# Kernel tuning notes

Measured on AMD Instinct MI355X. Metric: run time of the kernel, lower is better.

The kernel has to match this reference:

```python
import jax, jax.numpy as jnp
import numpy as np

N_NODES = 100000
N_EDGES = 1600000
IN_DIM, HID_DIM, OUT_DIM = 128, 128, 64


def setup_inputs() -> dict:
    key = jax.random.key(0)
    k1, k2, k3, k4 = jax.random.split(key, 4)
    x = jax.random.normal(k1, (N_NODES, IN_DIM), dtype=jnp.float32)
    edge_index = jax.random.randint(k2, (2, N_EDGES), 0, N_NODES, dtype=jnp.int64)
    # Glorot-ish init for weights, zeros for biases (as in PyG GCNConv defaults)
    W1 = jax.random.normal(k3, (IN_DIM, HID_DIM), dtype=jnp.float32) * (1.0 / np.sqrt(IN_DIM))
    b1 = jnp.zeros((HID_DIM,), dtype=jnp.float32)
    W2 = jax.random.normal(k4, (HID_DIM, OUT_DIM), dtype=jnp.float32) * (1.0 / np.sqrt(HID_DIM))
    b2 = jnp.zeros((OUT_DIM,), dtype=jnp.float32)
    return {"x": x, "edge_index": edge_index, "W1": W1, "b1": b1, "W2": W2, "b2": b2}


def _build_norm(edge_index, num_nodes):
    """Add self-loops and compute symmetric GCN normalization per edge.
    Returns (src, dst, norm) with self-loops appended."""
    loops = jnp.arange(num_nodes, dtype=edge_index.dtype)
    src = jnp.concatenate([edge_index[0], loops])
    dst = jnpp_concat = jnp.concatenate([edge_index[1], loops])
    deg = jax.ops.segment_sum(jnp.ones_like(dst, dtype=jnp.float32), dst,
                              num_segments=num_nodes)
    dinv = jax.lax.rsqrt(deg)  # deg >= 1 due to self-loops
    norm = dinv[src] * dinv[dst]  # [E + N]
    return src, dst, norm


def _gcn_conv(h, W, b, src, dst, norm, num_nodes):
    h = h @ W                                   # [N, F_out]
    msg = h[src] * norm[:, None]                # gather + scale, [E+N, F_out]
    agg = jax.ops.segment_sum(msg, dst, num_segments=num_nodes)
    return agg + b


def reference(x, edge_index, W1, b1, W2, b2):
    num_nodes = x.shape[0]
    src, dst, norm = _build_norm(edge_index, num_nodes)
    h = jax.nn.relu(_gcn_conv(x, W1, b1, src, dst, norm, num_nodes))
    return _gcn_conv(h, W2, b2, src, dst, norm, num_nodes)
```

## Files before the change

### kernel.cpp

```cpp
#include <hip/hip_runtime.h>

#define NN 100000
#define NE 1600000
#define NB 782
#define NBPAD 1024
#define CAPB 3072
#define EPB 8192
#define NROWPAD 100096
#define DPAD 136
#define OPAD 72

typedef __attribute__((ext_vector_type(8))) short short8;
typedef __attribute__((ext_vector_type(4))) float f32x4;

__device__ __forceinline__ unsigned short bf16rn(float f) {
    unsigned u = __float_as_uint(f);
    return (unsigned short)((u + 0x7FFFu + ((u >> 16) & 1u)) >> 16);
}
__device__ __forceinline__ float4 bf2x4(uint2 g) {
    float4 r;
    r.x = __uint_as_float(g.x << 16);
    r.y = __uint_as_float(g.x & 0xFFFF0000u);
    r.z = __uint_as_float(g.y << 16);
    r.w = __uint_as_float(g.y & 0xFFFF0000u);
    return r;
}
__device__ __forceinline__ uint2 packbf4(float4 v) {
    uint2 u;
    u.x = (unsigned)bf16rn(v.x) | ((unsigned)bf16rn(v.y) << 16);
    u.y = (unsigned)bf16rn(v.z) | ((unsigned)bf16rn(v.w) << 16);
    return u;
}

__global__ void detect_i64_k(const unsigned* __restrict__ ei, int* __restrict__ flag) {
    unsigned w = ei[2 * threadIdx.x + 1];
    unsigned long long b = __ballot(w == 0u);
    if (threadIdx.x == 0) *flag = (b == 0xFFFFFFFFFFFFFFFFull) ? 1 : 0;
}
__device__ __forceinline__ int load_node(const void* ei, int i64, long long idx) {
    return i64 ? (int)((const long long*)ei)[idx] : ((const int*)ei)[idx];
}

__global__ void cast_bf16_k(const float* __restrict__ in, ushort* __restrict__ outb,
                            long long n4) {
    long long i = (long long)blockIdx.x * 256 + threadIdx.x;
    if (i >= n4) return;
    ((uint2*)outb)[i] = packbf4(((const float4*)in)[i]);
}

__global__ void prep_wt_k(const float* __restrict__ W1, const float* __restrict__ W2,
                          ushort* __restrict__ W1t, ushort* __restrict__ W2t) {
    int i = blockIdx.x * 256 + threadIdx.x;
    if (i < 128 * 128) {
        int k = i >> 7, n = i & 127;
        W1t[n * 128 + k] = bf16rn(W1[k * 128 + n]);
    }
    if (i < 128 * 64) {
        int k = i >> 6, n = i & 63;
        W2t[n * 128 + k] = bf16rn(W2[k * 64 + n]);
    }
}

__global__ __launch_bounds__(256) void binfill_k(const void* __restrict__ ei,
                                                 const int* __restrict__ flag,
                                                 int* __restrict__ cur,
                                                 unsigned* __restrict__ bstage) {
    __shared__ unsigned binned[EPB];
    __shared__ int lcnt[NBPAD];
    __shared__ int lpos[NBPAD];
    __shared__ int gbase[NBPAD];
    __shared__ int tsum[256];
    int tid = threadIdx.x;
    long long e0 = (long long)blockIdx.x * EPB;
    int i64 = *flag;

    for (int i = tid; i < NBPAD; i += 256) lcnt[i] = 0;
    __syncthreads();

    for (int i = tid; i < EPB; i += 256) {
        long long e = e0 + i;
        if (e < NE) {
            int d = load_node(ei, i64, (long long)NE + e);
            atomicAdd(&lcnt[d >> 7], 1);
        }
    }
    __syncthreads();

    int base = tid * 4;
    int c0 = lcnt[base], c1 = lcnt[base + 1], c2 = lcnt[base + 2], c3 = lcnt[base + 3];
    int s = c0 + c1 + c2 + c3;
    tsum[tid] = s;
    __syncthreads();
    for (int off = 1; off < 256; off <<= 1) {
        int v = (tid >= off) ? tsum[tid - off] : 0;
        __syncthreads();
        tsum[tid] += v;
        __syncthreads();
    }
    int excl = tsum[tid] - s;
    int p0 = excl, p1 = excl + c0, p2 = p1 + c1, p3 = p2 + c2;
    lcnt[base] = p0; lcnt[base + 1] = p1; lcnt[base + 2] = p2; lcnt[base + 3] = p3;
    lpos[base] = p0; lpos[base + 1] = p1; lpos[base + 2] = p2; lpos[base + 3] = p3;
    if (base < NB)     gbase[base]     = c0 ? atomicAdd(&cur[base], c0) : 0;
    if (base + 1 < NB) gbase[base + 1] = c1 ? atomicAdd(&cur[base + 1], c1) : 0;
    if (base + 2 < NB) gbase[base + 2] = c2 ? atomicAdd(&cur[base + 2], c2) : 0;
    if (base + 3 < NB) gbase[base + 3] = c3 ? atomicAdd(&cur[base + 3], c3) : 0;
    __syncthreads();

    for (int i = tid; i < EPB; i += 256) {
        long long e = e0 + i;
        if (e < NE) {
            int sv = load_node(ei, i64, e);
            int d  = load_node(ei, i64, (long long)NE + e);
            int b  = d >> 7;
            int p  = atomicAdd(&lpos[b], 1);
            binned[p] = ((unsigned)(d & 127) << 17) | (unsigned)sv;
        }
    }
    __syncthreads();

    for (int b = tid; b < NB; b += 256) {
        int start = lcnt[b], endp = lpos[b];
        int gb = gbase[b];
        unsigned* dst = bstage + (long long)b * CAPB;
        for (int k = start; k < endp; k++) {
            int go = gb + (k - start);
            if (go < CAPB) dst[go] = binned[k];
        }
    }
}

__global__ __launch_bounds__(256) void regroup_k(const int* __restrict__ cur,
                                                 const unsigned* __restrict__ bstage,
                                                 int* __restrict__ cnt,
                                                 int* __restrict__ rowstart,
                                                 int* __restrict__ grouped) {
    __shared__ unsigned stash[CAPB];
    __shared__ int lcnt[128], lofs[128], lpos[128], sc[128];
    int tid = threadIdx.x;
    int b = blockIdx.x;

    int total = cur[b];
    if (total > CAPB) total = CAPB;
    const unsigned* seg = bstage + (long long)b * CAPB;
    for (int i = tid; i < total; i += 256) stash[i] = seg[i];
    __syncthreads();

    if (tid < 128) { lcnt[tid] = 0; lpos[tid] = 0; }
    __syncthreads();
    for (int i = tid; i < total; i += 256)
        atomicAdd(&lcnt[stash[i] >> 17], 1);
    __syncthreads();

    if (tid < 128) sc[tid] = lcnt[tid];
    __syncthreads();
    for (int off = 1; off < 128; off <<= 1) {
        int v = 0;
        if (tid < 128 && tid >= off) v = sc[tid - off];
        __syncthreads();
        if (tid < 128) sc[tid] += v;
        __syncthreads();
    }
    if (tid < 128) {
        lofs[tid] = sc[tid] - lcnt[tid];
        int node = b * 128 + tid;
        if (node < NN) {
            cnt[node] = lcnt[tid];
            rowstart[node] = b * CAPB + lofs[tid];
        }
    }
    __syncthreads();

    int* g = grouped + b * CAPB;
    for (int i = tid; i < total; i += 256) {
        unsigned e = stash[i];
        int nl = e >> 17;
        int p = atomicAdd(&lpos[nl], 1);
        g[lofs[nl] + p] = (int)(e & 0x1FFFFu);
    }
}

template <int LPN, bool BIAS, bool OUTB>
__global__ __launch_bounds__(256) void pull_bf16_k(const int* __restrict__ grouped,
                                                   const int* __restrict__ rowstart,
                                                   const int* __restrict__ cnt,
                                                   const ushort* __restrict__ hb,
                                                   const float* __restrict__ bias,
                                                   void* __restrict__ out) {
    int tid = threadIdx.x;
    int node = blockIdx.x * (256 / LPN) + tid / LPN;
    int lane = tid % LPN;
    if (node >= NN) return;

    const uint2* h2 = (const uint2*)hb;
    int deg = cnt[node];
    float di = rsqrtf((float)(deg + 1));
    float w0 = di * di;
    float4 hv = bf2x4(h2[(long long)node * LPN + lane]);
    float4 a0 = make_float4(hv.x * w0, hv.y * w0, hv.z * w0, hv.w * w0);
    float4 a1 = make_float4(0.f, 0.f, 0.f, 0.f);
    float4 a2 = make_float4(0.f, 0.f, 0.f, 0.f);
    float4 a3 = make_float4(0.f, 0.f, 0.f, 0.f);

    const int* row = grouped + rowstart[node];
    int j = 0;
    for (; j + 3 < deg; j += 4) {
        int s0 = row[j], s1 = row[j + 1], s2 = row[j + 2], s3 = row[j + 3];
        float q0 = rsqrtf((float)(cnt[s0] + 1)) * di;
        float q1 = rsqrtf((float)(cnt[s1] + 1)) * di;
        float q2 = rsqrtf((float)(cnt[s2] + 1)) * di;
        float q3 = rsqrtf((float)(cnt[s3] + 1)) * di;
        float4 v0 = bf2x4(h2[(long long)s0 * LPN + lane]);
        float4 v1 = bf2x4(h2[(long long)s1 * LPN + lane]);
        float4 v2 = bf2x4(h2[(long long)s2 * LPN + lane]);
        float4 v3 = bf2x4(h2[(long long)s3 * LPN + lane]);
        a0.x = fmaf(v0.x, q0, a0.x); a0.y = fmaf(v0.y, q0, a0.y);
        a0.z = fmaf(v0.z, q0, a0.z); a0.w = fmaf(v0.w, q0, a0.w);
        a1.x = fmaf(v1.x, q1, a1.x); a1.y = fmaf(v1.y, q1, a1.y);
        a1.z = fmaf(v1.z, q1, a1.z); a1.w = fmaf(v1.w, q1, a1.w);
        a2.x = fmaf(v2.x, q2, a2.x); a2.y = fmaf(v2.y, q2, a2.y);
        a2.z = fmaf(v2.z, q2, a2.z); a2.w = fmaf(v2.w, q2, a2.w);
        a3.x = fmaf(v3.x, q3, a3.x); a3.y = fmaf(v3.y, q3, a3.y);
        a3.z = fmaf(v3.z, q3, a3.z); a3.w = fmaf(v3.w, q3, a3.w);
    }
    for (; j < deg; j++) {
        int s0 = row[j];
        float q0 = rsqrtf((float)(cnt[s0] + 1)) * di;
        float4 v0 = bf2x4(h2[(long long)s0 * LPN + lane]);
        a0.x = fmaf(v0.x, q0, a0.x); a0.y = fmaf(v0.y, q0, a0.y);
        a0.z = fmaf(v0.z, q0, a0.z); a0.w = fmaf(v0.w, q0, a0.w);
    }
    a0.x += a1.x + a2.x + a3.x; a0.y += a1.y + a2.y + a3.y;
    a0.z += a1.z + a2.z + a3.z; a0.w += a1.w + a2.w + a3.w;
    if (BIAS) {
        float4 bb = ((const float4*)bias)[lane];
        a0.x += bb.x; a0.y += bb.y; a0.z += bb.z; a0.w += bb.w;
    }
    if (OUTB)
        ((uint2*)out)[(long long)node * LPN + lane] = packbf4(a0);
    else
        ((float4*)out)[(long long)node * LPN + lane] = a0;
}

__global__ __launch_bounds__(256) void dgemm_mfma_k(const ushort* __restrict__ Ab,
                                                    const ushort* __restrict__ W1t,
                                                    const float* __restrict__ b1,
                                                    const ushort* __restrict__ W2t,
                                                    ushort* __restrict__ H2b) {
    __shared__ ushort Tt[4][32 * DPAD];
    __shared__ ushort Ot[4][32 * OPAD];
    int tid = threadIdx.x;
    int wv = tid >> 6, lane = tid & 63;
    int m16 = lane & 15, quad = lane >> 4;
    int row0 = blockIdx.x * 128 + wv * 32;

    short8 af[2][4];
#pragma unroll
    for (int mt = 0; mt < 2; mt++)
#pragma unroll
        for (int kc = 0; kc < 4; kc++)
            af[mt][kc] = *(const short8*)(Ab + (long long)(row0 + mt * 16 + m16) * 128
                                          + kc * 32 + quad * 8);
    f32x4 accA[2][8];
#pragma unroll
    for (int mt = 0; mt < 2; mt++)
#pragma unroll
        for (int nt = 0; nt < 8; nt++) accA[mt][nt] = (f32x4){0.f, 0.f, 0.f, 0.f};

#pragma unroll
    for (int nt = 0; nt < 8; nt++) {
#pragma unroll
        for (int kc = 0; kc < 4; kc++) {
            short8 bf = *(const short8*)(W1t + (nt * 16 + m16) * 128 + kc * 32 + quad * 8);
            accA[0][nt] = __builtin_amdgcn_mfma_f32_16x16x32_bf16(af[0][kc], bf, accA[0][nt], 0, 0, 0);
            accA[1][nt] = __builtin_amdgcn_mfma_f32_16x16x32_bf16(af[1][kc], bf, accA[1][nt], 0, 0, 0);
        }
    }

#pragma unroll
    for (int nt = 0; nt < 8; nt++) {
        float bb = b1[nt * 16 + m16];
#pragma unroll
        for (int mt = 0; mt < 2; mt++)
#pragma unroll
            for (int r = 0; r < 4; r++) {
                float v = fmaxf(accA[mt][nt][r] + bb, 0.f);
                Tt[wv][(mt * 16 + quad * 4 + r) * DPAD + nt * 16 + m16] = bf16rn(v);
            }
    }
    __syncthreads();

    f32x4 accB[2][4];
#pragma unroll
    for (int mt = 0; mt < 2; mt++)
#pragma unroll
        for (int nt = 0; nt < 4; nt++) accB[mt][nt] = (f32x4){0.f, 0.f, 0.f, 0.f};

#pragma unroll
    for (int nt = 0; nt < 4; nt++) {
#pragma unroll
        for (int kc = 0; kc < 4; kc++) {
            short8 bf = *(const short8*)(W2t + (nt * 16 + m16) * 128 + kc * 32 + quad * 8);
#pragma unroll
            for (int mt = 0; mt < 2; mt++) {
                short8 aT = *(const short8*)(&Tt[wv][(mt * 16 + m16) * DPAD + kc * 32 + quad * 8]);
                accB[mt][nt] = __builtin_amdgcn_mfma_f32_16x16x32_bf16(aT, bf, accB[mt][nt], 0, 0, 0);
            }
        }
    }

#pragma unroll
    for (int nt = 0; nt < 4; nt++)
#pragma unroll
        for (int mt = 0; mt < 2; mt++)
#pragma unroll
            for (int r = 0; r < 4; r++)
                Ot[wv][(mt * 16 + quad * 4 + r) * OPAD + nt * 16 + m16] = bf16rn(accB[mt][nt][r]);
    __syncthreads();

    uint4* H4 = (uint4*)H2b;
#pragma unroll
    for (int it = 0; it < 4; it++) {
        int idx = it * 64 + lane;
        int r = idx >> 3, c = idx & 7;
        int grow = row0 + r;
        if (grow < NN) {
            uint4 v = *(const uint4*)(&Ot[wv][r * OPAD + c * 8]);
            H4[(long long)grow * 8 + c] = v;
        }
    }
}

extern "C" void kernel_launch(void* const* d_in, const int* in_sizes, int n_in,
                              void* d_out, int out_size, void* d_ws, size_t ws_size,
                              hipStream_t stream) {
    const float* x  = (const float*)d_in[0];
    const void*  ei = d_in[1];
    const float* W1 = (const float*)d_in[2];
    const float* b1 = (const float*)d_in[3];
    const float* W2 = (const float*)d_in[4];
    const float* b2 = (const float*)d_in[5];
    float* out = (float*)d_out;
    char* ws = (char*)d_ws;

    int*      flag     = (int*)ws;
    int*      cur      = (int*)(ws + 0x1000);
    int*      cnt      = (int*)(ws + 0x10000);
    int*      rowstart = (int*)(ws + 0x80000);
    unsigned* bstage   = (unsigned*)(ws + 0x100000);
    int*      grouped  = (int*)(ws + 0xB00000);
    ushort*   xb       = (ushort*)(ws + 0x1500000);
    ushort*   aggxb    = (ushort*)(ws + 0x2F00000);
    ushort*   h2b      = (ushort*)(ws + 0x4800000);
    ushort*   W1t      = (ushort*)(ws + 0x5500000);
    ushort*   W2t      = (ushort*)(ws + 0x5510000);

    hipMemsetAsync(cur, 0, NB * sizeof(int), stream);
    detect_i64_k<<<1, 64, 0, stream>>>((const unsigned*)ei, flag);
    cast_bf16_k<<<(NN * 32 + 255) / 256, 256, 0, stream>>>(x, xb, (long long)NN * 32);
    prep_wt_k<<<64, 256, 0, stream>>>(W1, W2, W1t, W2t);
    binfill_k<<<(NE + EPB - 1) / EPB, 256, 0, stream>>>(ei, flag, cur, bstage);
    regroup_k<<<NB, 256, 0, stream>>>(cur, bstage, cnt, rowstart, grouped);

    pull_bf16_k<32, false, true><<<(NN + 7) / 8, 256, 0, stream>>>(grouped, rowstart, cnt,
                                                                   xb, nullptr, aggxb);
    dgemm_mfma_k<<<NROWPAD / 128, 256, 0, stream>>>(aggxb, W1t, b1, W2t, h2b);

    pull_bf16_k<16, true, false><<<(NN + 15) / 16, 256, 0, stream>>>(grouped, rowstart, cnt,
                                                                     h2b, b2, out);
}
```

Before: 303.2 us.

## Precompute per-edge norm in CSR and widen pull gathers to 16 bytes

The adjacency now stores (src, norm) pairs per edge. A new kernel fills in each edge's norm once from a dinv array computed in regroup, so the pull kernels no longer do a dependent cnt[src] gather plus rsqrt per edge in both layers. The pull kernels load 8 bf16 values per lane with uint4 (half the lanes per node), use two accumulator sets, prefetch the next edge batch, and read the edge list with nontemporal loads. The cost is an extra kernel launch and edge storage that doubles from 4 to 8 bytes per entry.

```diff
diff --git a/kernel.cpp b/kernel.cpp
--- a/kernel.cpp
+++ b/kernel.cpp
@@ -17,19 +17,31 @@
     unsigned u = __float_as_uint(f);
     return (unsigned short)((u + 0x7FFFu + ((u >> 16) & 1u)) >> 16);
 }
-__device__ __forceinline__ float4 bf2x4(uint2 g) {
-    float4 r;
-    r.x = __uint_as_float(g.x << 16);
-    r.y = __uint_as_float(g.x & 0xFFFF0000u);
-    r.z = __uint_as_float(g.y << 16);
-    r.w = __uint_as_float(g.y & 0xFFFF0000u);
-    return r;
-}
 __device__ __forceinline__ uint2 packbf4(float4 v) {
     uint2 u;
     u.x = (unsigned)bf16rn(v.x) | ((unsigned)bf16rn(v.y) << 16);
     u.y = (unsigned)bf16rn(v.z) | ((unsigned)bf16rn(v.w) << 16);
     return u;
+}
+__device__ __forceinline__ unsigned packbf2(float x, float y) {
+    return (unsigned)bf16rn(x) | ((unsigned)bf16rn(y) << 16);
+}
+__device__ __forceinline__ void bf8acc(float* a, uint4 v, float q) {
+    a[0] = fmaf(__uint_as_float(v.x << 16), q, a[0]);
+    a[1] = fmaf(__uint_as_float(v.x & 0xFFFF0000u), q, a[1]);
+    a[2] = fmaf(__uint_as_float(v.y << 16), q, a[2]);
+    a[3] = fmaf(__uint_as_float(v.y & 0xFFFF0000u), q, a[3]);
+    a[4] = fmaf(__uint_as_float(v.z << 16), q, a[4]);
+    a[5] = fmaf(__uint_as_float(v.z & 0xFFFF0000u), q, a[5]);
+    a[6] = fmaf(__uint_as_float(v.w << 16), q, a[6]);
+    a[7] = fmaf(__uint_as_float(v.w & 0xFFFF0000u), q, a[7]);
+}
+__device__ __forceinline__ uint2 ldnt2(const unsigned long long* p) {
+    unsigned long long v = __builtin_nontemporal_load(p);
+    uint2 r;
+    r.x = (unsigned)v;
+    r.y = (unsigned)(v >> 32);
+    return r;
 }
 
 __global__ void detect_i64_k(const unsigned* __restrict__ ei, int* __restrict__ flag) {
@@ -134,7 +146,8 @@
                                                  const unsigned* __restrict__ bstage,
                                                  int* __restrict__ cnt,
                                                  int* __restrict__ rowstart,
-                                                 int* __restrict__ grouped) {
+                                                 uint2* __restrict__ g2,
+                                                 float* __restrict__ dinv) {
     __shared__ unsigned stash[CAPB];
     __shared__ int lcnt[128], lofs[128], lpos[128], sc[128];
     int tid = threadIdx.x;
@@ -167,79 +180,116 @@
         if (node < NN) {
             cnt[node] = lcnt[tid];
             rowstart[node] = b * CAPB + lofs[tid];
-        }
-    }
-    __syncthreads();
-
-    int* g = grouped + b * CAPB;
+            dinv[node] = rsqrtf((float)(lcnt[tid] + 1));
+        }
+    }
+    __syncthreads();
+
+    uint2* g = g2 + (long long)b * CAPB;
     for (int i = tid; i < total; i += 256) {
         unsigned e = stash[i];
         int nl = e >> 17;
         int p = atomicAdd(&lpos[nl], 1);
-        g[lofs[nl] + p] = (int)(e & 0x1FFFFu);
-    }
+        g[lofs[nl] + p] = make_uint2(e & 0x1FFFFu, (unsigned)(b * 128 + nl));
+    }
+}
+
+__global__ __launch_bounds__(256) void qn_k(const int* __restrict__ cur,
+                                            const float* __restrict__ dinv,
+                                            uint2* __restrict__ g2) {
+    int b = blockIdx.x;
+    int total = cur[b];
+    if (total > CAPB) total = CAPB;
+    uint2* g = g2 + (long long)b * CAPB;
+    for (int i = threadIdx.x; i < total; i += 256) {
+        uint2 e = g[i];
+        float q = dinv[e.x] * dinv[e.y];
+        g[i] = make_uint2(e.x, __float_as_uint(q));
+    }
+}
+
+template <int LPN>
+__device__ __forceinline__ void gf4(const uint4* __restrict__ h4, int lane,
+                                    uint2 e0, uint2 e1, uint2 e2, uint2 e3,
+                                    float* a, float* b) {
+    uint4 v0 = h4[e0.x * LPN + lane];
+    uint4 v1 = h4[e1.x * LPN + lane];
+    uint4 v2 = h4[e2.x * LPN + lane];
+    uint4 v3 = h4[e3.x * LPN + lane];
+    bf8acc(a, v0, __uint_as_float(e0.y));
+    bf8acc(b, v1, __uint_as_float(e1.y));
+    bf8acc(a, v2, __uint_as_float(e2.y));
+    bf8acc(b, v3, __uint_as_float(e3.y));
 }
 
 template <int LPN, bool BIAS, bool OUTB>
-__global__ __launch_bounds__(256) void pull_bf16_k(const int* __restrict__ grouped,
-                                                   const int* __restrict__ rowstart,
-                                                   const int* __restrict__ cnt,
-                                                   const ushort* __restrict__ hb,
-                                                   const float* __restrict__ bias,
-                                                   void* __restrict__ out) {
+__global__ __launch_bounds__(256) void pull2_k(const uint2* __restrict__ g2,
+                                               const int* __restrict__ rowstart,
+                                               const int* __restrict__ cnt,
+                                               const float* __restrict__ dinv,
+                                               const ushort* __restrict__ hb,
+                                               const float* __restrict__ bias,
+                                               void* __restrict__ out) {
     int tid = threadIdx.x;
     int node = blockIdx.x * (256 / LPN) + tid / LPN;
-    int lane = tid % LPN;
+    int lane = tid & (LPN - 1);
     if (node >= NN) return;
 
-    const uint2* h2 = (const uint2*)hb;
+    const uint4* h4 = (const uint4*)hb;
+    float di = dinv[node];
+    float w0 = di * di;
+    float a[8] = {0.f, 0.f, 0.f, 0.f, 0.f, 0.f, 0.f, 0.f};
+    float b[8] = {0.f, 0.f, 0.f, 0.f, 0.f, 0.f, 0.f, 0.f};
+    bf8acc(a, h4[(unsigned)node * LPN + lane], w0);
+
     int deg = cnt[node];
-    float di = rsqrtf((float)(deg + 1));
-    float w0 = di * di;
-    float4 hv = bf2x4(h2[(long long)node * LPN + lane]);
-    float4 a0 = make_float4(hv.x * w0, hv.y * w0, hv.z * w0, hv.w * w0);
-    float4 a1 = make_float4(0.f, 0.f, 0.f, 0.f);
-    float4 a2 = make_float4(0.f, 0.f, 0.f, 0.f);
-    float4 a3 = make_float4(0.f, 0.f, 0.f, 0.f);
-
-    const int* row = grouped + rowstart[node];
+    const unsigned long long* rowq =
+        (const unsigned long long*)(g2 + rowstart[node]);
+
     int j = 0;
-    for (; j + 3 < deg; j += 4) {
-        int s0 = row[j], s1 = row[j + 1], s2 = row[j + 2], s3 = row[j + 3];
-        float q0 = rsqrtf((float)(cnt[s0] + 1)) * di;
-        float q1 = rsqrtf((float)(cnt[s1] + 1)) * di;
-        float q2 = rsqrtf((float)(cnt[s2] + 1)) * di;
-        float q3 = rsqrtf((float)(cnt[s3] + 1)) * di;
-        float4 v0 = bf2x4(h2[(long long)s0 * LPN + lane]);
-        float4 v1 = bf2x4(h2[(long long)s1 * LPN + lane]);
-        float4 v2 = bf2x4(h2[(long long)s2 * LPN + lane]);
-        float4 v3 = bf2x4(h2[(long long)s3 * LPN + lane]);
-        a0.x = fmaf(v0.x, q0, a0.x); a0.y = fmaf(v0.y, q0, a0.y);
-        a0.z = fmaf(v0.z, q0, a0.z); a0.w = fmaf(v0.w, q0, a0.w);
-        a1.x = fmaf(v1.x, q1, a1.x); a1.y = fmaf(v1.y, q1, a1.y);
-        a1.z = fmaf(v1.z, q1, a1.z); a1.w = fmaf(v1.w, q1, a1.w);
-        a2.x = fmaf(v2.x, q2, a2.x); a2.y = fmaf(v2.y, q2, a2.y);
-        a2.z = fmaf(v2.z, q2, a2.z); a2.w = fmaf(v2.w, q2, a2.w);
-        a3.x = fmaf(v3.x, q3, a3.x); a3.y = fmaf(v3.y, q3, a3.y);
-        a3.z = fmaf(v3.z, q3, a3.z); a3.w = fmaf(v3.w, q3, a3.w);
+    if (deg >= 8) {
+        uint2 e0 = ldnt2(rowq + 0), e1 = ldnt2(rowq + 1);
+        uint2 e2 = ldnt2(rowq + 2), e3 = ldnt2(rowq + 3);
+        for (; j + 7 < deg; j += 4) {
+            uint2 f0 = ldnt2(rowq + j + 4), f1 = ldnt2(rowq + j + 5);
+            uint2 f2 = ldnt2(rowq + j + 6), f3 = ldnt2(rowq + j + 7);
+            gf4<LPN>(h4, lane, e0, e1, e2, e3, a, b);
+            e0 = f0; e1 = f1; e2 = f2; e3 = f3;
+        }
+        gf4<LPN>(h4, lane, e0, e1, e2, e3, a, b);
+        j += 4;
+    } else if (deg >= 4) {
+        gf4<LPN>(h4, lane, ldnt2(rowq + 0), ldnt2(rowq + 1),
+                 ldnt2(rowq + 2), ldnt2(rowq + 3), a, b);
+        j = 4;
     }
     for (; j < deg; j++) {
-        int s0 = row[j];
-        float q0 = rsqrtf((float)(cnt[s0] + 1)) * di;
-        float4 v0 = bf2x4(h2[(long long)s0 * LPN + lane]);
-        a0.x = fmaf(v0.x, q0, a0.x); a0.y = fmaf(v0.y, q0, a0.y);
-        a0.z = fmaf(v0.z, q0, a0.z); a0.w = fmaf(v0.w, q0, a0.w);
-    }
-    a0.x += a1.x + a2.x + a3.x; a0.y += a1.y + a2.y + a3.y;
-    a0.z += a1.z + a2.z + a3.z; a0.w += a1.w + a2.w + a3.w;
+        uint2 e = ldnt2(rowq + j);
+        bf8acc(a, h4[e.x * LPN + lane], __uint_as_float(e.y));
+    }
+
+    float o[8];
+#pragma unroll
+    for (int k = 0; k < 8; k++) o[k] = a[k] + b[k];
     if (BIAS) {
-        float4 bb = ((const float4*)bias)[lane];
-        a0.x += bb.x; a0.y += bb.y; a0.z += bb.z; a0.w += bb.w;
-    }
-    if (OUTB)
-        ((uint2*)out)[(long long)node * LPN + lane] = packbf4(a0);
-    else
-        ((float4*)out)[(long long)node * LPN + lane] = a0;
+        float4 b0 = ((const float4*)bias)[2 * lane];
+        float4 b1 = ((const float4*)bias)[2 * lane + 1];
+        o[0] += b0.x; o[1] += b0.y; o[2] += b0.z; o[3] += b0.w;
+        o[4] += b1.x; o[5] += b1.y; o[6] += b1.z; o[7] += b1.w;
+    }
+    if (OUTB) {
+        uint4 p;
+        p.x = packbf2(o[0], o[1]);
+        p.y = packbf2(o[2], o[3]);
+        p.z = packbf2(o[4], o[5]);
+        p.w = packbf2(o[6], o[7]);
+        ((uint4*)out)[(unsigned)node * LPN + lane] = p;
+    } else {
+        float4 lo = make_float4(o[0], o[1], o[2], o[3]);
+        float4 hi = make_float4(o[4], o[5], o[6], o[7]);
+        ((float4*)out)[(unsigned)node * (2 * LPN) + 2 * lane] = lo;
+        ((float4*)out)[(unsigned)node * (2 * LPN) + 2 * lane + 1] = hi;
+    }
 }
 
 __global__ __launch_bounds__(256) void dgemm_mfma_k(const ushort* __restrict__ Ab,
@@ -348,24 +398,26 @@
     int*      cnt      = (int*)(ws + 0x10000);
     int*      rowstart = (int*)(ws + 0x80000);
     unsigned* bstage   = (unsigned*)(ws + 0x100000);
-    int*      grouped  = (int*)(ws + 0xB00000);
-    ushort*   xb       = (ushort*)(ws + 0x1500000);
-    ushort*   aggxb    = (ushort*)(ws + 0x2F00000);
-    ushort*   h2b      = (ushort*)(ws + 0x4800000);
-    ushort*   W1t      = (ushort*)(ws + 0x5500000);
-    ushort*   W2t      = (ushort*)(ws + 0x5510000);
+    uint2*    g2       = (uint2*)(ws + 0xB00000);
+    ushort*   xb       = (ushort*)(ws + 0x1E00000);
+    ushort*   aggxb    = (ushort*)(ws + 0x3700000);
+    ushort*   h2b      = (ushort*)(ws + 0x5000000);
+    ushort*   W1t      = (ushort*)(ws + 0x5D00000);
+    ushort*   W2t      = (ushort*)(ws + 0x5D10000);
+    float*    dinv     = (float*)(ws + 0x5D20000);
 
     hipMemsetAsync(cur, 0, NB * sizeof(int), stream);
     detect_i64_k<<<1, 64, 0, stream>>>((const unsigned*)ei, flag);
     cast_bf16_k<<<(NN * 32 + 255) / 256, 256, 0, stream>>>(x, xb, (long long)NN * 32);
     prep_wt_k<<<64, 256, 0, stream>>>(W1, W2, W1t, W2t);
     binfill_k<<<(NE + EPB - 1) / EPB, 256, 0, stream>>>(ei, flag, cur, bstage);
-    regroup_k<<<NB, 256, 0, stream>>>(cur, bstage, cnt, rowstart, grouped);
-
-    pull_bf16_k<32, false, true><<<(NN + 7) / 8, 256, 0, stream>>>(grouped, rowstart, cnt,
-                                                                   xb, nullptr, aggxb);
+    regroup_k<<<NB, 256, 0, stream>>>(cur, bstage, cnt, rowstart, g2, dinv);
+    qn_k<<<NB, 256, 0, stream>>>(cur, dinv, g2);
+
+    pull2_k<16, false, true><<<(NN + 15) / 16, 256, 0, stream>>>(g2, rowstart, cnt, dinv,
+                                                                 xb, nullptr, aggxb);
     dgemm_mfma_k<<<NROWPAD / 128, 256, 0, stream>>>(aggxb, W1t, b1, W2t, h2b);
 
-    pull_bf16_k<16, true, false><<<(NN + 15) / 16, 256, 0, stream>>>(grouped, rowstart, cnt,
-                                                                     h2b, b2, out);
-}
+    pull2_k<8, true, false><<<(NN + 31) / 32, 256, 0, stream>>>(g2, rowstart, cnt, dinv,
+                                                                h2b, b2, out);
+}
```

Measured after the change: 335.0 us. 10.5% more time.
